# Kernel tuning notes

Measured on AMD Instinct MI355X. Metric: run time of the kernel, lower is better.

Reference implementation:

```python
import jax, jax.numpy as jnp
import numpy as np

LN_EPS = 1e-5
L2_EPS = 1e-12  # torch F.normalize eps


def _layernorm(h, g, b):
    mu = jnp.mean(h, axis=-1, keepdims=True)
    var = jnp.var(h, axis=-1, keepdims=True)
    return (h - mu) * jax.lax.rsqrt(var + LN_EPS) * g + b


def _l2norm(h):
    n = jnp.linalg.norm(h, axis=-1, keepdims=True)
    return h / jnp.maximum(n, L2_EPS)


def _temperature(epoch, total_epochs):
    warmup = total_epochs * 0.1
    if epoch < warmup:
        return 2.0
    progress = (epoch - warmup) / (total_epochs - warmup)
    return max(0.7, 2.0 - 1.3 * progress)


def setup_inputs() -> dict:
    key = jax.random.key(0)
    ks = jax.random.split(key, 4)
    B, T, D, P, C = 8, 4096, 1024, 512, 64
    x = jax.random.normal(ks[0], (B, T, D), dtype=jnp.float32)
    w1 = jax.random.normal(ks[1], (D, C), dtype=jnp.float32) * 0.02
    b1 = jnp.zeros((C,), jnp.float32)
    ln1_g = jnp.ones((C,), jnp.float32)
    ln1_b = jnp.zeros((C,), jnp.float32)
    patterns = jax.random.normal(ks[2], (P, C), dtype=jnp.float32)
    patterns = _l2norm(patterns)  # init is row-orthonormalized in torch via SVD; unit rows suffice
    w2 = jax.random.normal(ks[3], (C, D), dtype=jnp.float32) * 0.02
    b2 = jnp.zeros((D,), jnp.float32)
    ln2_g = jnp.ones((D,), jnp.float32)
    ln2_b = jnp.zeros((D,), jnp.float32)
    return {"x": x, "w1": w1, "b1": b1, "ln1_g": ln1_g, "ln1_b": ln1_b,
            "patterns": patterns, "w2": w2, "b2": b2, "ln2_g": ln2_g, "ln2_b": ln2_b,
            "epoch": 0, "total_epochs": 100}


def reference(x, w1, b1, ln1_g, ln1_b, patterns, w2, b2, ln2_g, ln2_b, epoch, total_epochs):
    n_patterns = patterns.shape[0]
    # bottleneck projection + LayerNorm: [B,T,D] -> [B,T,C]
    Q = _layernorm(jnp.einsum('btd,dc->btc', x, w1) + b1, ln1_g, ln1_b)
    Q_norm = _l2norm(Q)
    K_norm = _l2norm(patterns)  # [P,C]
    temp = _temperature(epoch, total_epochs)
    logits = jnp.einsum('btc,pc->btp', Q_norm, K_norm) / temp  # [B,T,P]
    hard_indices = jnp.argmax(logits, axis=-1)  # [B,T]
    assignments = jax.nn.one_hot(hard_indices, n_patterns, dtype=jnp.float32)  # eval: hard
    pattern_emb_low = jnp.einsum('btp,pc->btc', assignments, patterns)
    pattern_emb = _layernorm(jnp.einsum('btc,cd->btd', pattern_emb_low, w2) + b2, ln2_g, ln2_b)
    return (pattern_emb, assignments, logits, hard_indices, Q)
```

## Files before the change

### kernel.cpp

```cpp
#include <hip/hip_runtime.h>

#define O_PE 0
#define O_AS 33554432
#define O_LG 50331648
#define O_HI 67108864
#define O_Q  67141632

__global__ void k0_pre(const float* __restrict__ patterns, const float* __restrict__ w2,
                       const float* __restrict__ b2, const float* __restrict__ ln2g,
                       const float* __restrict__ ln2b, const int* __restrict__ epoch,
                       const int* __restrict__ total_epochs,
                       float* __restrict__ invt, float* __restrict__ knT,
                       float* __restrict__ peb) {
  const int b = blockIdx.x, t = threadIdx.x;
  __shared__ float pat[64];
  __shared__ float red[8];

  if (b == 0 && t == 0) {
    float ep = (float)epoch[0], te = (float)total_epochs[0];
    float warm = te * 0.1f;
    float temp;
    if (ep < warm) temp = 2.0f;
    else {
      float prog = (ep - warm) / (te - warm);
      temp = fmaxf(0.7f, 2.0f - 1.3f * prog);
    }
    invt[0] = 1.0f / temp;
  }

  if (t < 64) pat[t] = patterns[b * 64 + t];
  __syncthreads();

  if (t < 64) {
    float v = pat[t];
    float s = v * v;
    #pragma unroll
    for (int m = 1; m < 64; m <<= 1) s += __shfl_xor(s, m);
    float scale = 1.0f / fmaxf(sqrtf(s), 1e-12f);
    knT[(size_t)t * 512 + b] = v * scale;
  }

  const int d0 = t * 4;
  float4 acc = *(const float4*)&b2[d0];
  #pragma unroll 8
  for (int k = 0; k < 64; ++k) {
    float pk = pat[k];
    float4 w = *(const float4*)&w2[(size_t)k * 1024 + d0];
    acc.x = fmaf(pk, w.x, acc.x);
    acc.y = fmaf(pk, w.y, acc.y);
    acc.z = fmaf(pk, w.z, acc.z);
    acc.w = fmaf(pk, w.w, acc.w);
  }
  float s1 = acc.x + acc.y + acc.z + acc.w;
  float s2 = acc.x*acc.x + acc.y*acc.y + acc.z*acc.z + acc.w*acc.w;
  #pragma unroll
  for (int m = 1; m < 64; m <<= 1) { s1 += __shfl_xor(s1, m); s2 += __shfl_xor(s2, m); }
  const int wid = t >> 6;
  if ((t & 63) == 0) { red[wid] = s1; red[wid + 4] = s2; }
  __syncthreads();
  s1 = red[0] + red[1] + red[2] + red[3];
  s2 = red[4] + red[5] + red[6] + red[7];
  float mu = s1 * (1.0f / 1024.0f);
  float var = s2 * (1.0f / 1024.0f) - mu * mu;
  float rstd = rsqrtf(var + 1e-5f);
  float4 g  = *(const float4*)&ln2g[d0];
  float4 bb = *(const float4*)&ln2b[d0];
  float4 o;
  o.x = (acc.x - mu) * rstd * g.x + bb.x;
  o.y = (acc.y - mu) * rstd * g.y + bb.y;
  o.z = (acc.z - mu) * rstd * g.z + bb.z;
  o.w = (acc.w - mu) * rstd * g.w + bb.w;
  *(float4*)&peb[(size_t)b * 1024 + d0] = o;
}

__global__ __launch_bounds__(256) void k_fused(
    const float* __restrict__ x, const float* __restrict__ w1,
    const float* __restrict__ b1, const float* __restrict__ ln1g,
    const float* __restrict__ ln1b, const float* __restrict__ knT,
    const float* __restrict__ invtp, const float* __restrict__ peb,
    float* __restrict__ outPe, float* __restrict__ outAs,
    float* __restrict__ outLg, float* __restrict__ outHi,
    float* __restrict__ outQ) {
  __shared__ float smem[16896];
  const int tid = threadIdx.x;
  const int rowbase = blockIdx.x * 64;

  const int g  = tid >> 6;
  const int t  = tid & 63;
  const int rt = t >> 3, ct = t & 7;
  const int r0 = rt * 8, c0 = ct * 8;
  const int kbase = g * 256;

  float* xsT = smem;
  float* w1s = smem + 8704;

  float acc[8][8];
  #pragma unroll
  for (int i = 0; i < 8; ++i)
    #pragma unroll
    for (int j = 0; j < 8; ++j) acc[i][j] = 0.f;

  const float* xp = x + (size_t)(rowbase + (t >> 3)) * 1024 + kbase + (t & 7) * 4;
  const int wkr = t >> 4;
  const int wc4 = (t & 15) * 4;

  for (int kt = 0; kt < 8; ++kt) {
    const int kb = kt * 32;
    float4 xv[8], wv[8];
    #pragma unroll
    for (int p = 0; p < 8; ++p)
      xv[p] = *(const float4*)(xp + (size_t)p * 8192 + kb);
    const float* wp = w1 + (size_t)(kbase + kb + wkr) * 64 + wc4;
    #pragma unroll
    for (int p = 0; p < 8; ++p)
      wv[p] = *(const float4*)(wp + (size_t)p * 256);
    __syncthreads();
    #pragma unroll
    for (int p = 0; p < 8; ++p) {
      const int row = (t >> 3) + 8 * p;
      const int kc4 = (t & 7) * 4;
      xsT[g*2176 + (kc4+0)*68 + row] = xv[p].x;
      xsT[g*2176 + (kc4+1)*68 + row] = xv[p].y;
      xsT[g*2176 + (kc4+2)*68 + row] = xv[p].z;
      xsT[g*2176 + (kc4+3)*68 + row] = xv[p].w;
    }
    #pragma unroll
    for (int p = 0; p < 8; ++p)
      *(float4*)&w1s[g*2048 + (wkr + 4*p)*64 + wc4] = wv[p];
    __syncthreads();
    #pragma unroll 4
    for (int kk = 0; kk < 32; ++kk) {
      float4 a0 = *(float4*)&xsT[g*2176 + kk*68 + r0];
      float4 a1 = *(float4*)&xsT[g*2176 + kk*68 + r0 + 4];
      float4 b0 = *(float4*)&w1s[g*2048 + kk*64 + c0];
      float4 b1v = *(float4*)&w1s[g*2048 + kk*64 + c0 + 4];
      float av[8] = {a0.x, a0.y, a0.z, a0.w, a1.x, a1.y, a1.z, a1.w};
      float bv[8] = {b0.x, b0.y, b0.z, b0.w, b1v.x, b1v.y, b1v.z, b1v.w};
      #pragma unroll
      for (int i = 0; i < 8; ++i)
        #pragma unroll
        for (int j = 0; j < 8; ++j)
          acc[i][j] = fmaf(av[i], bv[j], acc[i][j]);
    }
  }

  __syncthreads();
  if (g > 0) {
    float* hc = smem + (g - 1) * 4096;
    #pragma unroll
    for (int i = 0; i < 8; ++i) {
      float4 v0, v1;
      v0.x = acc[i][0]; v0.y = acc[i][1]; v0.z = acc[i][2]; v0.w = acc[i][3];
      v1.x = acc[i][4]; v1.y = acc[i][5]; v1.z = acc[i][6]; v1.w = acc[i][7];
      *(float4*)&hc[(r0+i)*64 + c0]     = v0;
      *(float4*)&hc[(r0+i)*64 + c0 + 4] = v1;
    }
  }
  __syncthreads();
  float* qns = smem + 12288;
  if (g == 0) {
    float bb[8], gg[8], ee[8];
    {
      float4 t0 = *(const float4*)&b1[c0];
      float4 t1 = *(const float4*)&b1[c0 + 4];
      float4 t2 = *(const float4*)&ln1g[c0];
      float4 t3 = *(const float4*)&ln1g[c0 + 4];
      float4 t4 = *(const float4*)&ln1b[c0];
      float4 t5 = *(const float4*)&ln1b[c0 + 4];
      bb[0]=t0.x; bb[1]=t0.y; bb[2]=t0.z; bb[3]=t0.w; bb[4]=t1.x; bb[5]=t1.y; bb[6]=t1.z; bb[7]=t1.w;
      gg[0]=t2.x; gg[1]=t2.y; gg[2]=t2.z; gg[3]=t2.w; gg[4]=t3.x; gg[5]=t3.y; gg[6]=t3.z; gg[7]=t3.w;
      ee[0]=t4.x; ee[1]=t4.y; ee[2]=t4.z; ee[3]=t4.w; ee[4]=t5.x; ee[5]=t5.y; ee[6]=t5.z; ee[7]=t5.w;
    }
    #pragma unroll
    for (int i = 0; i < 8; ++i) {
      const int row = r0 + i;
      float h[8];
      #pragma unroll
      for (int j = 0; j < 8; ++j) h[j] = acc[i][j] + bb[j];
      #pragma unroll
      for (int gg2 = 0; gg2 < 3; ++gg2) {
        float4 p0 = *(float4*)&smem[gg2*4096 + row*64 + c0];
        float4 p1 = *(float4*)&smem[gg2*4096 + row*64 + c0 + 4];
        h[0] += p0.x; h[1] += p0.y; h[2] += p0.z; h[3] += p0.w;
        h[4] += p1.x; h[5] += p1.y; h[6] += p1.z; h[7] += p1.w;
      }
      float s1 = 0.f, s2 = 0.f;
      #pragma unroll
      for (int j = 0; j < 8; ++j) { s1 += h[j]; s2 += h[j]*h[j]; }
      #pragma unroll
      for (int m = 1; m < 8; m <<= 1) { s1 += __shfl_xor(s1, m); s2 += __shfl_xor(s2, m); }
      const float mu   = s1 * 0.015625f;
      const float var  = s2 * 0.015625f - mu * mu;
      const float rstd = rsqrtf(var + 1e-5f);
      float q[8]; float t2s = 0.f;
      #pragma unroll
      for (int j = 0; j < 8; ++j) { q[j] = (h[j] - mu) * rstd * gg[j] + ee[j]; t2s += q[j]*q[j]; }
      #pragma unroll
      for (int m = 1; m < 8; m <<= 1) t2s += __shfl_xor(t2s, m);
      const float scl = 1.0f / fmaxf(sqrtf(t2s), 1e-12f);
      float4 qa, qc;
      qa.x = q[0]; qa.y = q[1]; qa.z = q[2]; qa.w = q[3];
      qc.x = q[4]; qc.y = q[5]; qc.z = q[6]; qc.w = q[7];
      *(float4*)&outQ[(size_t)(rowbase + row) * 64 + c0]     = qa;
      *(float4*)&outQ[(size_t)(rowbase + row) * 64 + c0 + 4] = qc;
      #pragma unroll
      for (int j = 0; j < 8; ++j) qns[row*68 + c0 + j] = q[j] * scl;
    }
  }

  const float invt = invtp[0];
  const int pt  = tid & 15;
  const int rt2 = tid >> 4;
  float* kns = smem;
  int* sidx = (int*)(smem + 16640);

  float bm[4]; int bi[4];
  #pragma unroll
  for (int i = 0; i < 4; ++i) { bm[i] = -3.0e38f; bi[i] = 0; }

  for (int ch = 0; ch < 4; ++ch) {
    __syncthreads();
    #pragma unroll
    for (int p = 0; p < 8; ++p) {
      const int id = tid + p * 256;
      const int cr = id >> 5, pc = (id & 31) * 4;
      *(float4*)&kns[cr*132 + pc] = *(const float4*)&knT[(size_t)cr * 512 + ch * 128 + pc];
    }
    __syncthreads();

    float a2[4][8];
    #pragma unroll
    for (int i = 0; i < 4; ++i)
      #pragma unroll
      for (int j = 0; j < 8; ++j) a2[i][j] = 0.f;

    #pragma unroll 2
    for (int cb = 0; cb < 16; ++cb) {
      float qv[4][4];
      #pragma unroll
      for (int i = 0; i < 4; ++i) {
        float4 tq = *(float4*)&qns[(rt2 + 16*i)*68 + cb*4];
        qv[i][0] = tq.x; qv[i][1] = tq.y; qv[i][2] = tq.z; qv[i][3] = tq.w;
      }
      #pragma unroll
      for (int dc = 0; dc < 4; ++dc) {
        float4 k0 = *(float4*)&kns[(cb*4+dc)*132 + pt*8];
        float4 k1 = *(float4*)&kns[(cb*4+dc)*132 + pt*8 + 4];
        float kv[8] = {k0.x, k0.y, k0.z, k0.w, k1.x, k1.y, k1.z, k1.w};
        #pragma unroll
        for (int i = 0; i < 4; ++i)
          #pragma unroll
          for (int j = 0; j < 8; ++j)
            a2[i][j] = fmaf(qv[i][dc], kv[j], a2[i][j]);
      }
    }

    #pragma unroll
    for (int i = 0; i < 4; ++i) {
      const size_t row = (size_t)(rowbase + rt2 + 16*i);
      float v[8];
      #pragma unroll
      for (int j = 0; j < 8; ++j) v[j] = a2[i][j] * invt;
      const int pb = ch * 128 + pt * 8;
      #pragma unroll
      for (int j = 0; j < 8; ++j)
        if (v[j] > bm[i]) { bm[i] = v[j]; bi[i] = pb + j; }
      float4 o0, o1;
      o0.x = v[0]; o0.y = v[1]; o0.z = v[2]; o0.w = v[3];
      o1.x = v[4]; o1.y = v[5]; o1.z = v[6]; o1.w = v[7];
      *(float4*)&outLg[row * 512 + pb]     = o0;
      *(float4*)&outLg[row * 512 + pb + 4] = o1;
    }
  }

  #pragma unroll
  for (int i = 0; i < 4; ++i) {
    #pragma unroll
    for (int m = 1; m < 16; m <<= 1) {
      float ov = __shfl_xor(bm[i], m);
      int   oi = __shfl_xor(bi[i], m);
      if (ov > bm[i] || (ov == bm[i] && oi < bi[i])) { bm[i] = ov; bi[i] = oi; }
    }
    if (pt == 0) {
      sidx[rt2 + 16*i] = bi[i];
      outHi[rowbase + rt2 + 16*i] = (float)bi[i];
    }
  }
  __syncthreads();

  #pragma unroll
  for (int p = 0; p < 32; ++p) {
    const int id = tid + p * 256;
    const int r = id >> 7, c4 = (id & 127) * 4;
    const int b = sidx[r];
    float4 z; z.x = 0.f; z.y = 0.f; z.z = 0.f; z.w = 0.f;
    if (b >= c4 && b < c4 + 4) ((float*)&z)[b - c4] = 1.0f;
    *(float4*)&outAs[(size_t)(rowbase + r) * 512 + c4] = z;
  }

  const float4* peb4 = (const float4*)peb;
  float4* o4 = (float4*)outPe;
  #pragma unroll 4
  for (int p = 0; p < 64; ++p) {
    const int id = tid + p * 256;
    const int r = id >> 8, c4 = id & 255;
    o4[(size_t)(rowbase + r) * 256 + c4] = peb4[(size_t)sidx[r] * 256 + c4];
  }
}

extern "C" void kernel_launch(void* const* d_in, const int* in_sizes, int n_in,
                              void* d_out, int out_size, void* d_ws, size_t ws_size,
                              hipStream_t stream) {
  (void)in_sizes; (void)n_in; (void)out_size; (void)ws_size;
  const float* x        = (const float*)d_in[0];
  const float* w1       = (const float*)d_in[1];
  const float* b1       = (const float*)d_in[2];
  const float* ln1g     = (const float*)d_in[3];
  const float* ln1b     = (const float*)d_in[4];
  const float* patterns = (const float*)d_in[5];
  const float* w2       = (const float*)d_in[6];
  const float* b2       = (const float*)d_in[7];
  const float* ln2g     = (const float*)d_in[8];
  const float* ln2b     = (const float*)d_in[9];
  const int*   epoch    = (const int*)d_in[10];
  const int*   total    = (const int*)d_in[11];

  float* out = (float*)d_out;
  float* outPe = out + O_PE;
  float* outAs = out + O_AS;
  float* outLg = out + O_LG;
  float* outHi = out + O_HI;
  float* outQ  = out + O_Q;

  float* wsf  = (float*)d_ws;
  float* invt = wsf;
  float* knT  = wsf + 64;
  float* peb  = (float*)((char*)d_ws + 131328);

  hipLaunchKernelGGL(k0_pre, dim3(512), dim3(256), 0, stream,
                     patterns, w2, b2, ln2g, ln2b, epoch, total, invt, knT, peb);
  hipLaunchKernelGGL(k_fused, dim3(512), dim3(256), 0, stream,
                     x, w1, b1, ln1g, ln1b, knT, invt, peb,
                     outPe, outAs, outLg, outHi, outQ);
}
```

Baseline: 159.8 us.

## Swizzle GEMM1 LDS tiles and restructure logits GEMM to read patterns directly

The first GEMM's transposed x tile in LDS gets an XOR swizzle on the row index, and the w1 tile is padded to a stride of 68 to cut LDS bank conflicts. The logits stage is restructured so each wave owns 128 patterns, accumulates 16 rows by 8 patterns per thread, and reads knT straight from global/L2 instead of staging four chunks through LDS with a sync per chunk. The argmax is now reduced across lanes and then across waves through shared memory. Launch bounds now request 2 blocks per CU, and the 128-entry accumulator raises register pressure, which may cause spills.

```diff
diff --git a/kernel.cpp b/kernel.cpp
--- a/kernel.cpp
+++ b/kernel.cpp
@@ -73,7 +73,7 @@
   *(float4*)&peb[(size_t)b * 1024 + d0] = o;
 }
 
-__global__ __launch_bounds__(256) void k_fused(
+__global__ __launch_bounds__(256, 2) void k_fused(
     const float* __restrict__ x, const float* __restrict__ w1,
     const float* __restrict__ b1, const float* __restrict__ ln1g,
     const float* __restrict__ ln1b, const float* __restrict__ knT,
@@ -81,7 +81,7 @@
     float* __restrict__ outPe, float* __restrict__ outAs,
     float* __restrict__ outLg, float* __restrict__ outHi,
     float* __restrict__ outQ) {
-  __shared__ float smem[16896];
+  __shared__ float smem[17408];
   const int tid = threadIdx.x;
   const int rowbase = blockIdx.x * 64;
 
@@ -115,25 +115,29 @@
     for (int p = 0; p < 8; ++p)
       wv[p] = *(const float4*)(wp + (size_t)p * 256);
     __syncthreads();
-    #pragma unroll
-    for (int p = 0; p < 8; ++p) {
-      const int row = (t >> 3) + 8 * p;
+    {
       const int kc4 = (t & 7) * 4;
-      xsT[g*2176 + (kc4+0)*68 + row] = xv[p].x;
-      xsT[g*2176 + (kc4+1)*68 + row] = xv[p].y;
-      xsT[g*2176 + (kc4+2)*68 + row] = xv[p].z;
-      xsT[g*2176 + (kc4+3)*68 + row] = xv[p].w;
+      const int sw = 8 * ((kc4 >> 3) & 3);
+      #pragma unroll
+      for (int p = 0; p < 8; ++p) {
+        const int row = ((t >> 3) + 8 * p) ^ sw;
+        xsT[g*2176 + (kc4+0)*68 + row] = xv[p].x;
+        xsT[g*2176 + (kc4+1)*68 + row] = xv[p].y;
+        xsT[g*2176 + (kc4+2)*68 + row] = xv[p].z;
+        xsT[g*2176 + (kc4+3)*68 + row] = xv[p].w;
+      }
     }
     #pragma unroll
     for (int p = 0; p < 8; ++p)
-      *(float4*)&w1s[g*2048 + (wkr + 4*p)*64 + wc4] = wv[p];
+      *(float4*)&w1s[g*2176 + (wkr + 4*p)*68 + wc4] = wv[p];
     __syncthreads();
     #pragma unroll 4
     for (int kk = 0; kk < 32; ++kk) {
-      float4 a0 = *(float4*)&xsT[g*2176 + kk*68 + r0];
-      float4 a1 = *(float4*)&xsT[g*2176 + kk*68 + r0 + 4];
-      float4 b0 = *(float4*)&w1s[g*2048 + kk*64 + c0];
-      float4 b1v = *(float4*)&w1s[g*2048 + kk*64 + c0 + 4];
+      const int rb = r0 ^ (8 * ((kk >> 3) & 3));
+      float4 a0 = *(float4*)&xsT[g*2176 + kk*68 + rb];
+      float4 a1 = *(float4*)&xsT[g*2176 + kk*68 + rb + 4];
+      float4 b0 = *(float4*)&w1s[g*2176 + kk*68 + c0];
+      float4 b1v = *(float4*)&w1s[g*2176 + kk*68 + c0 + 4];
       float av[8] = {a0.x, a0.y, a0.z, a0.w, a1.x, a1.y, a1.z, a1.w};
       float bv[8] = {b0.x, b0.y, b0.z, b0.w, b1v.x, b1v.y, b1v.z, b1v.w};
       #pragma unroll
@@ -207,84 +211,82 @@
       for (int j = 0; j < 8; ++j) qns[row*68 + c0 + j] = q[j] * scl;
     }
   }
+  __syncthreads();
 
   const float invt = invtp[0];
-  const int pt  = tid & 15;
-  const int rt2 = tid >> 4;
-  float* kns = smem;
-  int* sidx = (int*)(smem + 16640);
-
-  float bm[4]; int bi[4];
-  #pragma unroll
-  for (int i = 0; i < 4; ++i) { bm[i] = -3.0e38f; bi[i] = 0; }
-
-  for (int ch = 0; ch < 4; ++ch) {
-    __syncthreads();
-    #pragma unroll
-    for (int p = 0; p < 8; ++p) {
-      const int id = tid + p * 256;
-      const int cr = id >> 5, pc = (id & 31) * 4;
-      *(float4*)&kns[cr*132 + pc] = *(const float4*)&knT[(size_t)cr * 512 + ch * 128 + pc];
-    }
-    __syncthreads();
-
-    float a2[4][8];
-    #pragma unroll
-    for (int i = 0; i < 4; ++i)
-      #pragma unroll
-      for (int j = 0; j < 8; ++j) a2[i][j] = 0.f;
-
-    #pragma unroll 2
-    for (int cb = 0; cb < 16; ++cb) {
-      float qv[4][4];
-      #pragma unroll
-      for (int i = 0; i < 4; ++i) {
-        float4 tq = *(float4*)&qns[(rt2 + 16*i)*68 + cb*4];
-        qv[i][0] = tq.x; qv[i][1] = tq.y; qv[i][2] = tq.z; qv[i][3] = tq.w;
-      }
-      #pragma unroll
-      for (int dc = 0; dc < 4; ++dc) {
-        float4 k0 = *(float4*)&kns[(cb*4+dc)*132 + pt*8];
-        float4 k1 = *(float4*)&kns[(cb*4+dc)*132 + pt*8 + 4];
-        float kv[8] = {k0.x, k0.y, k0.z, k0.w, k1.x, k1.y, k1.z, k1.w};
+  const int lane = tid & 63;
+  const int w    = tid >> 6;
+  const int brt  = lane & 3;
+  const int pt16 = lane >> 2;
+  const int pbase = w * 128 + pt16 * 8;
+
+  float* avm = smem;
+  int*   avi = (int*)(smem + 256);
+  int*   sidx = (int*)(smem + 512);
+
+  float a2[16][8];
+  #pragma unroll
+  for (int i = 0; i < 16; ++i)
+    #pragma unroll
+    for (int j = 0; j < 8; ++j) a2[i][j] = 0.f;
+
+  for (int cb = 0; cb < 16; ++cb) {
+    float kv[4][8];
+    #pragma unroll
+    for (int dc = 0; dc < 4; ++dc) {
+      float4 k0 = *(const float4*)&knT[(size_t)(cb*4+dc)*512 + pbase];
+      float4 k1 = *(const float4*)&knT[(size_t)(cb*4+dc)*512 + pbase + 4];
+      kv[dc][0]=k0.x; kv[dc][1]=k0.y; kv[dc][2]=k0.z; kv[dc][3]=k0.w;
+      kv[dc][4]=k1.x; kv[dc][5]=k1.y; kv[dc][6]=k1.z; kv[dc][7]=k1.w;
+    }
+    #pragma unroll
+    for (int i = 0; i < 16; ++i) {
+      float4 qv = *(float4*)&qns[(brt + 4*i)*68 + cb*4];
+      float qq[4] = {qv.x, qv.y, qv.z, qv.w};
+      #pragma unroll
+      for (int dc = 0; dc < 4; ++dc)
         #pragma unroll
-        for (int i = 0; i < 4; ++i)
-          #pragma unroll
-          for (int j = 0; j < 8; ++j)
-            a2[i][j] = fmaf(qv[i][dc], kv[j], a2[i][j]);
-      }
-    }
-
-    #pragma unroll
-    for (int i = 0; i < 4; ++i) {
-      const size_t row = (size_t)(rowbase + rt2 + 16*i);
-      float v[8];
-      #pragma unroll
-      for (int j = 0; j < 8; ++j) v[j] = a2[i][j] * invt;
-      const int pb = ch * 128 + pt * 8;
-      #pragma unroll
-      for (int j = 0; j < 8; ++j)
-        if (v[j] > bm[i]) { bm[i] = v[j]; bi[i] = pb + j; }
-      float4 o0, o1;
-      o0.x = v[0]; o0.y = v[1]; o0.z = v[2]; o0.w = v[3];
-      o1.x = v[4]; o1.y = v[5]; o1.z = v[6]; o1.w = v[7];
-      *(float4*)&outLg[row * 512 + pb]     = o0;
-      *(float4*)&outLg[row * 512 + pb + 4] = o1;
-    }
-  }
-
-  #pragma unroll
-  for (int i = 0; i < 4; ++i) {
-    #pragma unroll
-    for (int m = 1; m < 16; m <<= 1) {
-      float ov = __shfl_xor(bm[i], m);
-      int   oi = __shfl_xor(bi[i], m);
-      if (ov > bm[i] || (ov == bm[i] && oi < bi[i])) { bm[i] = ov; bi[i] = oi; }
-    }
-    if (pt == 0) {
-      sidx[rt2 + 16*i] = bi[i];
-      outHi[rowbase + rt2 + 16*i] = (float)bi[i];
-    }
+        for (int j = 0; j < 8; ++j)
+          a2[i][j] = fmaf(qq[dc], kv[dc][j], a2[i][j]);
+    }
+  }
+
+  #pragma unroll
+  for (int i = 0; i < 16; ++i) {
+    const int row = brt + 4*i;
+    const size_t grow = (size_t)(rowbase + row);
+    float v[8];
+    float bm = -3.0e38f; int bi = 0;
+    #pragma unroll
+    for (int j = 0; j < 8; ++j) {
+      v[j] = a2[i][j] * invt;
+      if (v[j] > bm) { bm = v[j]; bi = pbase + j; }
+    }
+    float4 o0, o1;
+    o0.x = v[0]; o0.y = v[1]; o0.z = v[2]; o0.w = v[3];
+    o1.x = v[4]; o1.y = v[5]; o1.z = v[6]; o1.w = v[7];
+    *(float4*)&outLg[grow * 512 + pbase]     = o0;
+    *(float4*)&outLg[grow * 512 + pbase + 4] = o1;
+    #pragma unroll
+    for (int m = 4; m < 64; m <<= 1) {
+      float ov = __shfl_xor(bm, m);
+      int   oi = __shfl_xor(bi, m);
+      if (ov > bm || (ov == bm && oi < bi)) { bm = ov; bi = oi; }
+    }
+    if (pt16 == 0) { avm[w*64 + row] = bm; avi[w*64 + row] = bi; }
+  }
+  __syncthreads();
+
+  if (tid < 64) {
+    float bm = avm[tid]; int bi = avi[tid];
+    #pragma unroll
+    for (int w2 = 1; w2 < 4; ++w2) {
+      float m = avm[w2*64 + tid];
+      int   i = avi[w2*64 + tid];
+      if (m > bm) { bm = m; bi = i; }
+    }
+    sidx[tid] = bi;
+    outHi[rowbase + tid] = (float)bi;
   }
   __syncthreads();
 
```

Measured after the change: 165.8 us. 1.04x slower.
